# Kernel tuning notes

Measured on AMD Instinct MI355X. Metric: run time of the kernel, lower is better.

## Reference

```python
import jax, jax.numpy as jnp
import numpy as np

N_MOL = 2000      # number of molecules (subsystems)
MOL_SIZE = 64     # atoms per molecule (equal-sized, contiguous)
N_ATOMS = N_MOL * MOL_SIZE


def setup_inputs() -> dict:
    key = jax.random.key(0)
    positions = jax.random.normal(key, (N_ATOMS, 3), dtype=jnp.float32)
    # contiguous equal-sized molecules: atom a belongs to molecule a // MOL_SIZE
    atomic_subsystem_indices = (jnp.arange(N_ATOMS) // MOL_SIZE).astype(jnp.int32)
    return {"positions": positions,
            "atomic_subsystem_indices": atomic_subsystem_indices}


def _pair_indices():
    """All ordered intra-molecule pairs (i, j), j != i, for contiguous
    equal-sized molecules. Matches the order of the torch code's global
    all-pairs enumeration followed by the same-molecule mask filter:
    i ascending, then j ascending within i's molecule (skipping j == i)."""
    A = MOL_SIZE
    i_loc = jnp.repeat(jnp.arange(A), A - 1)                       # [A*(A-1)]
    off = jnp.arange(A - 1)
    # j_loc[i, k] = k if k < i else k + 1  (skip j == i)
    j_loc = (off[None, :] + (off[None, :] >= jnp.arange(A)[:, None]).astype(off.dtype)).reshape(-1)
    base = (jnp.arange(N_MOL) * A)[:, None]                        # [M, 1]
    i_idx = (base + i_loc[None, :]).reshape(-1)                    # [M*A*(A-1)]
    j_idx = (base + j_loc[None, :]).reshape(-1)
    return jnp.stack((i_idx, j_idx))                               # [2, P]


def reference(positions, atomic_subsystem_indices):
    # pair enumeration depends only on the (static) molecule layout
    pair_indices = _pair_indices()                                 # [2, P] int
    # gather both endpoints, subtract: r_ij = pos[j] - pos[i]
    r_ij = positions[pair_indices[1]] - positions[pair_indices[0]]  # [P, 3]
    d_ij = jnp.linalg.norm(r_ij, axis=1, keepdims=True)             # [P, 1]
    return pair_indices, d_ij, r_ij
```

## Files before the change

### kernel.cpp

```cpp
#include <hip/hip_runtime.h>


#define N_MOL   2000
#define MOL_A   64
#define PPM     (MOL_A * (MOL_A - 1))
#define P_TOTAL (N_MOL * PPM)

__global__ __launch_bounds__(256) void Pairlist_54932631716418_kernel(
    const float* __restrict__ pos, float* __restrict__ out) {
  const int p0 = (blockIdx.x * 256 + threadIdx.x) * 4;
  if (p0 >= P_TOTAL) return;
  const int m    = p0 / PPM;
  const int r0   = p0 - m * PPM;
  const int base = m * MOL_A;

  float fi[4], fj[4], fd[4], frx[4], fry[4], frz[4];
#pragma unroll
  for (int s = 0; s < 4; ++s) {
    const int r  = r0 + s;
    const int i  = r / 63;
    const int k  = r - i * 63;
    const int j  = k + (k >= i ? 1 : 0);
    const int gi = base + i;
    const int gj = base + j;
    const float xi = pos[3 * gi + 0];
    const float yi = pos[3 * gi + 1];
    const float zi = pos[3 * gi + 2];
    const float xj = pos[3 * gj + 0];
    const float yj = pos[3 * gj + 1];
    const float zj = pos[3 * gj + 2];
    const float rx = xj - xi, ry = yj - yi, rz = zj - zi;
    fi[s]  = (float)gi;
    fj[s]  = (float)gj;
    frx[s] = rx; fry[s] = ry; frz[s] = rz;
    fd[s]  = sqrtf(rx * rx + ry * ry + rz * rz);
  }

  *(float4*)(out + p0)               = make_float4(fi[0], fi[1], fi[2], fi[3]);
  *(float4*)(out + P_TOTAL + p0)     = make_float4(fj[0], fj[1], fj[2], fj[3]);
  *(float4*)(out + 2 * P_TOTAL + p0) = make_float4(fd[0], fd[1], fd[2], fd[3]);
  float4* orr = (float4*)(out + 3 * P_TOTAL + 3 * p0);
  orr[0] = make_float4(frx[0], fry[0], frz[0], frx[1]);
  orr[1] = make_float4(fry[1], frz[1], frx[2], fry[2]);
  orr[2] = make_float4(frz[2], frx[3], fry[3], frz[3]);
}

extern "C" void kernel_launch(void* const* d_in, const int* in_sizes, int n_in,
                              void* d_out, int out_size, void* d_ws, size_t ws_size,
                              hipStream_t stream) {
  const float* pos = (const float*)d_in[0];
  float* out = (float*)d_out;
  const int nthread = P_TOTAL / 4;
  const int blocks  = nthread / 256;
  Pairlist_54932631716418_kernel<<<blocks, 256, 0, stream>>>(pos, out);
}
```

Measured before the change: 195.2 us.

## Stage positions in LDS and coalesce r_ij stores via shared transpose

Each block now loads the positions of the (at most two) molecules it covers into shared memory once and reads endpoint coordinates from there, replacing scattered global gathers. The r_ij vectors are written to a padded shared buffer, then stored cooperatively so consecutive threads write consecutive float4s. The aim is fewer redundant global loads and fully coalesced output writes. The cost is two block barriers and extra LDS traffic. The kernel is write-bandwidth bound, so the gain may be small.

```diff
diff --git a/kernel.cpp b/kernel.cpp
--- a/kernel.cpp
+++ b/kernel.cpp
@@ -5,44 +5,76 @@
 #define MOL_A   64
 #define PPM     (MOL_A * (MOL_A - 1))
 #define P_TOTAL (N_MOL * PPM)
+#define BLOCK   256
+#define PPB     1024
+#define POS_W   384
+#define RSTRIDE 13
 
-__global__ __launch_bounds__(256) void Pairlist_54932631716418_kernel(
+__global__ __launch_bounds__(BLOCK) void Pairlist_54932631716418_kernel(
     const float* __restrict__ pos, float* __restrict__ out) {
-  const int p0 = (blockIdx.x * 256 + threadIdx.x) * 4;
-  if (p0 >= P_TOTAL) return;
-  const int m    = p0 / PPM;
-  const int r0   = p0 - m * PPM;
-  const int base = m * MOL_A;
+  __shared__ float posb[POS_W];
+  __shared__ float rbuf[BLOCK * RSTRIDE];
 
-  float fi[4], fj[4], fd[4], frx[4], fry[4], frz[4];
+  const int t  = threadIdx.x;
+  const int P0 = blockIdx.x * PPB;
+  const int mf = P0 / PPM;
+
+  {
+    const int gmax = N_MOL * MOL_A * 3 - 1;
+    int g0 = mf * (MOL_A * 3);
+    int a0 = g0 + t;       if (a0 > gmax) a0 = gmax;
+    posb[t] = pos[a0];
+    if (t + BLOCK < POS_W) {
+      int a1 = g0 + t + BLOCK; if (a1 > gmax) a1 = gmax;
+      posb[t + BLOCK] = pos[a1];
+    }
+  }
+  __syncthreads();
+
+  const int p0 = P0 + 4 * t;
+  int rp     = p0 - mf * PPM;
+  int molOff = 0;
+  int base   = mf * MOL_A;
+  if (rp >= PPM) { rp -= PPM; molOff = MOL_A * 3; base += MOL_A; }
+
+  float fi[4], fj[4], fd[4];
 #pragma unroll
   for (int s = 0; s < 4; ++s) {
-    const int r  = r0 + s;
-    const int i  = r / 63;
-    const int k  = r - i * 63;
-    const int j  = k + (k >= i ? 1 : 0);
-    const int gi = base + i;
-    const int gj = base + j;
-    const float xi = pos[3 * gi + 0];
-    const float yi = pos[3 * gi + 1];
-    const float zi = pos[3 * gi + 2];
-    const float xj = pos[3 * gj + 0];
-    const float yj = pos[3 * gj + 1];
-    const float zj = pos[3 * gj + 2];
+    const int r = rp + s;
+    const int i = r / 63;
+    const int k = r - 63 * i;
+    const int j = k + (k >= i ? 1 : 0);
+    const float xi = posb[molOff + 3 * i + 0];
+    const float yi = posb[molOff + 3 * i + 1];
+    const float zi = posb[molOff + 3 * i + 2];
+    const float xj = posb[molOff + 3 * j + 0];
+    const float yj = posb[molOff + 3 * j + 1];
+    const float zj = posb[molOff + 3 * j + 2];
     const float rx = xj - xi, ry = yj - yi, rz = zj - zi;
-    fi[s]  = (float)gi;
-    fj[s]  = (float)gj;
-    frx[s] = rx; fry[s] = ry; frz[s] = rz;
-    fd[s]  = sqrtf(rx * rx + ry * ry + rz * rz);
+    fi[s] = (float)(base + i);
+    fj[s] = (float)(base + j);
+    fd[s] = sqrtf(rx * rx + ry * ry + rz * rz);
+    rbuf[RSTRIDE * t + 3 * s + 0] = rx;
+    rbuf[RSTRIDE * t + 3 * s + 1] = ry;
+    rbuf[RSTRIDE * t + 3 * s + 2] = rz;
   }
 
   *(float4*)(out + p0)               = make_float4(fi[0], fi[1], fi[2], fi[3]);
   *(float4*)(out + P_TOTAL + p0)     = make_float4(fj[0], fj[1], fj[2], fj[3]);
   *(float4*)(out + 2 * P_TOTAL + p0) = make_float4(fd[0], fd[1], fd[2], fd[3]);
-  float4* orr = (float4*)(out + 3 * P_TOTAL + 3 * p0);
-  orr[0] = make_float4(frx[0], fry[0], frz[0], frx[1]);
-  orr[1] = make_float4(fry[1], frz[1], frx[2], fry[2]);
-  orr[2] = make_float4(frz[2], frx[3], fry[3], frz[3]);
+
+  __syncthreads();
+
+  float* outr = out + 3 * (size_t)P_TOTAL + 3 * (size_t)P0;
+#pragma unroll
+  for (int s = 0; s < 3; ++s) {
+    const int g = t + s * BLOCK;
+    const int a = g / 3;
+    const int b = g - 3 * a;
+    const int w = RSTRIDE * a + 4 * b;
+    float4 v = make_float4(rbuf[w], rbuf[w + 1], rbuf[w + 2], rbuf[w + 3]);
+    *(float4*)(outr + 4 * g) = v;
+  }
 }
 
 extern "C" void kernel_launch(void* const* d_in, const int* in_sizes, int n_in,
@@ -50,7 +82,6 @@
                               hipStream_t stream) {
   const float* pos = (const float*)d_in[0];
   float* out = (float*)d_out;
-  const int nthread = P_TOTAL / 4;
-  const int blocks  = nthread / 256;
-  Pairlist_54932631716418_kernel<<<blocks, 256, 0, stream>>>(pos, out);
+  const int blocks = P_TOTAL / PPB;
+  Pairlist_54932631716418_kernel<<<blocks, BLOCK, 0, stream>>>(pos, out);
 }
```

After: 190.3 us. -2.5%, faster.
